# Optimization experiments

Measured on AMD Instinct MI355X. Metric: run time of the kernel, lower is better.

Reference implementation:

```python
import jax, jax.numpy as jnp
import numpy as np

NA, NW = 131072, 131072
N = NA + NW
E = 1048576
R = 4
DIN = 64
H = 128
L = 2
EPS = 1e-5


def setup_inputs() -> dict:
    key = jax.random.key(0)
    ks = jax.random.split(key, 20)
    s_in = 1.0 / np.sqrt(DIN)
    s_h = 1.0 / np.sqrt(H)
    return {
        "x_assignments": jax.random.normal(ks[0], (NA, DIN), jnp.float32),
        "x_workers": jax.random.normal(ks[1], (NW, DIN), jnp.float32),
        "edge_index": jax.random.randint(ks[2], (2, E), 0, N),
        "edge_type": jax.random.randint(ks[3], (E,), 0, R),
        "W_in_a": jax.random.normal(ks[4], (DIN, H), jnp.float32) * s_in,
        "b_in_a": jnp.zeros((H,), jnp.float32),
        "W_in_w": jax.random.normal(ks[5], (DIN, H), jnp.float32) * s_in,
        "b_in_w": jnp.zeros((H,), jnp.float32),
        "W_rel": jax.random.normal(ks[6], (L, R, H, H), jnp.float32) * s_h,
        "W_root": jax.random.normal(ks[7], (L, H, H), jnp.float32) * s_h,
        "b_conv": jnp.zeros((L, H), jnp.float32),
        "ln_g": jnp.ones((L, H), jnp.float32),
        "ln_b": jnp.zeros((L, H), jnp.float32),
        "W_out": jax.random.normal(ks[8], (H, 1), jnp.float32) * s_h,
        "b_out": jnp.zeros((1,), jnp.float32),
        "base": jnp.zeros((), jnp.float32),
    }


def _layernorm(x, g, b):
    mu = jnp.mean(x, axis=-1, keepdims=True)
    var = jnp.var(x, axis=-1, keepdims=True)
    return (x - mu) * jax.lax.rsqrt(var + EPS) * g + b


def reference(x_assignments, x_workers, edge_index, edge_type,
              W_in_a, b_in_a, W_in_w, b_in_w,
              W_rel, W_root, b_conv, ln_g, ln_b,
              W_out, b_out, base):
    # type-specific input projection + relu, then flatten node space
    ha = jax.nn.relu(x_assignments @ W_in_a + b_in_a)
    hw = jax.nn.relu(x_workers @ W_in_w + b_in_w)
    h = jnp.concatenate([ha, hw], axis=0)  # [N, H]
    src, dst = edge_index[0], edge_index[1]
    for l in range(L):
        hs = h[src]  # [E, H] gathered source features
        out = h @ W_root[l] + b_conv[l]  # root transform + bias
        for r in range(R):
            m = (edge_type == r).astype(h.dtype)  # [E]
            agg = jax.ops.segment_sum(hs * m[:, None], dst, num_segments=N)
            cnt = jax.ops.segment_sum(m, dst, num_segments=N)
            mean = agg / jnp.maximum(cnt, 1.0)[:, None]  # per-relation mean aggr
            out = out + mean @ W_rel[l, r]
        h = jax.nn.relu(_layernorm(out, ln_g[l], ln_b[l]))
        # dropout inactive (eval mode)
    h_t = h[:NA]  # target node type slice (offset 0)
    pred = base + (h_t @ W_out + b_out)[:, 0]
    return pred
```

## Files before the change

### kernel.cpp

```cpp
#include <hip/hip_runtime.h>

#define NA_ 131072
#define NN  262144
#define EE  1048576
#define RR  4
#define EPS_ 1e-5f

typedef unsigned short ushort_t;
typedef unsigned char uchar_t;
typedef unsigned int uint_t;
typedef __attribute__((ext_vector_type(8))) short bf16x8;
typedef __attribute__((ext_vector_type(4))) float f32x4;

__device__ __forceinline__ float bf2f(uint_t u16) {
    return __uint_as_float(u16 << 16);
}
__device__ __forceinline__ uint_t f2bf(float f) {
    uint_t x = __float_as_uint(f);
    return (x + 0x7fffu + ((x >> 16) & 1u)) >> 16;
}

__device__ __forceinline__ void gl2lds16(const void* g, void* l) {
    __builtin_amdgcn_global_load_lds(
        (const __attribute__((address_space(1))) void*)g,
        (__attribute__((address_space(3))) void*)l, 16, 0, 0);
}

__global__ __launch_bounds__(256) void proj_gemm(const float* __restrict__ A,
                                                 const short* __restrict__ Btg,
                                                 const float* __restrict__ bias,
                                                 ushort_t* __restrict__ C) {
    const int K = 64;
    __shared__ short As[128][K + 8];
    __shared__ short Bs[128][K + 8];
    const int tid  = threadIdx.x;
    const int lane = tid & 63;
    const int l15  = lane & 15;
    const int q    = lane >> 4;
    const int wv   = tid >> 6;
    const int wr   = (wv >> 1) * 64;
    const int wc   = (wv & 1) * 64;
    const size_t blockRow = (size_t)blockIdx.x * 128;

    #pragma unroll
    for (int it = 0; it < 4; it++) {
        int sidx = (it * 256 + tid) * 8;
        int row = sidx / K, col = sidx % K;
        const float* Ag = A + (blockRow + row) * K + col;
        float4 v0 = *(const float4*)Ag;
        float4 v1 = *(const float4*)(Ag + 4);
        uint4 u;
        u.x = f2bf(v0.x) | (f2bf(v0.y) << 16);
        u.y = f2bf(v0.z) | (f2bf(v0.w) << 16);
        u.z = f2bf(v1.x) | (f2bf(v1.y) << 16);
        u.w = f2bf(v1.z) | (f2bf(v1.w) << 16);
        *(uint4*)&As[row][col] = u;
        *(uint4*)&Bs[row][col] = *(const uint4*)(Btg + (size_t)row * K + col);
    }
    __syncthreads();

    f32x4 acc[4][4];
    #pragma unroll
    for (int i = 0; i < 4; i++)
        #pragma unroll
        for (int j = 0; j < 4; j++) {
            acc[i][j][0] = 0.f; acc[i][j][1] = 0.f;
            acc[i][j][2] = 0.f; acc[i][j][3] = 0.f;
        }

    #pragma unroll
    for (int kk = 0; kk < 2; kk++) {
        bf16x8 af[4], bfr[4];
        #pragma unroll
        for (int i = 0; i < 4; i++)
            af[i] = *(const bf16x8*)&As[wr + i * 16 + l15][kk * 32 + q * 8];
        #pragma unroll
        for (int j = 0; j < 4; j++)
            bfr[j] = *(const bf16x8*)&Bs[wc + j * 16 + l15][kk * 32 + q * 8];
        #pragma unroll
        for (int i = 0; i < 4; i++)
            #pragma unroll
            for (int j = 0; j < 4; j++)
                acc[i][j] = __builtin_amdgcn_mfma_f32_16x16x32_bf16(
                    af[i], bfr[j], acc[i][j], 0, 0, 0);
    }

    #pragma unroll
    for (int j = 0; j < 4; j++) {
        int gcol = wc + j * 16 + l15;
        float bv = bias[gcol];
        #pragma unroll
        for (int i = 0; i < 4; i++) {
            size_t rbase = blockRow + wr + i * 16 + q * 4;
            #pragma unroll
            for (int r = 0; r < 4; r++) {
                float v = fmaxf(acc[i][j][r] + bv, 0.f);
                C[(rbase + r) * 128 + gcol] = (ushort_t)f2bf(v);
            }
        }
    }
}

__global__ void prep_weights(const float* __restrict__ Wia,
                             const float* __restrict__ Wiw,
                             const float* __restrict__ Wroot,
                             const float* __restrict__ Wrel,
                             short* __restrict__ wt) {
    int e = blockIdx.x * 256 + threadIdx.x;
    if (e < 8192) {
        int k = e >> 7, n = e & 127;
        wt[n * 64 + k] = (short)f2bf(Wia[e]);
    } else if (e < 16384) {
        int t = e - 8192;
        int k = t >> 7, n = t & 127;
        wt[8192 + n * 64 + k] = (short)f2bf(Wiw[t]);
    } else {
        int t = e - 16384;
        int l = t / 81920;
        int d = t % 81920;
        int kc = d / 16384;
        int rem2 = d % 16384;
        int n = rem2 >> 7;
        int kkk = rem2 & 127;
        float val = (kc < 4)
            ? Wrel[(((size_t)l * 4 + kc) * 128 + kkk) * 128 + n]
            : Wroot[((size_t)l * 128 + kkk) * 128 + n];
        wt[16384 + (size_t)l * 81920 + kc * 16384 + n * 128 + kkk] =
            (short)f2bf(val);
    }
}

__global__ void count_edges(const int* __restrict__ dstv,
                            const int* __restrict__ et,
                            uint_t* __restrict__ cntp,
                            uchar_t* __restrict__ rank) {
    int base = blockIdx.x * 1024 + threadIdx.x;
    int e0 = base, e1 = base + 256, e2 = base + 512, e3 = base + 768;
    int r0 = et[e0], r1 = et[e1], r2 = et[e2], r3 = et[e3];
    int d0 = dstv[e0], d1 = dstv[e1], d2 = dstv[e2], d3 = dstv[e3];
    uint_t o0 = atomicAdd(&cntp[d0], 1u << (8 * r0));
    uint_t o1 = atomicAdd(&cntp[d1], 1u << (8 * r1));
    uint_t o2 = atomicAdd(&cntp[d2], 1u << (8 * r2));
    uint_t o3 = atomicAdd(&cntp[d3], 1u << (8 * r3));
    rank[e0] = (uchar_t)((o0 >> (8 * r0)) & 0xffu);
    rank[e1] = (uchar_t)((o1 >> (8 * r1)) & 0xffu);
    rank[e2] = (uchar_t)((o2 >> (8 * r2)) & 0xffu);
    rank[e3] = (uchar_t)((o3 >> (8 * r3)) & 0xffu);
}

__global__ void inv_deg(uint_t* __restrict__ cntp, float* __restrict__ inv,
                        int* __restrict__ deg) {
    int i = blockIdx.x * 256 + threadIdx.x;
    if (i < NN) {
        uint_t c = cntp[i];
        int c0 = c & 255, c1 = (c >> 8) & 255, c2 = (c >> 16) & 255, c3 = c >> 24;
        inv[i]          = 1.0f / (float)(c0 > 1 ? c0 : 1);
        inv[NN + i]     = 1.0f / (float)(c1 > 1 ? c1 : 1);
        inv[2 * NN + i] = 1.0f / (float)(c2 > 1 ? c2 : 1);
        inv[3 * NN + i] = 1.0f / (float)(c3 > 1 ? c3 : 1);
        deg[i] = c0 + c1 + c2 + c3;
        cntp[i] = ((uint_t)c0 << 8) | ((uint_t)(c0 + c1) << 16)
                | ((uint_t)(c0 + c1 + c2) << 24);
    }
}

__global__ void scan1(const int* __restrict__ deg, int* __restrict__ offs,
                      int* __restrict__ bsum) {
    __shared__ int lds[256];
    int tid = threadIdx.x;
    int i = blockIdx.x * 256 + tid;
    int v = deg[i];
    int incl = v;
    lds[tid] = incl;
    __syncthreads();
    for (int off = 1; off < 256; off <<= 1) {
        int t = (tid >= off) ? lds[tid - off] : 0;
        __syncthreads();
        incl += t;
        lds[tid] = incl;
        __syncthreads();
    }
    offs[i] = incl - v;
    if (tid == 255) bsum[blockIdx.x] = incl;
}

__global__ void scan_bsum(int* __restrict__ bsum) {
    __shared__ int lds[256];
    int tid = threadIdx.x;
    int t0 = bsum[tid * 4 + 0], t1 = bsum[tid * 4 + 1];
    int t2 = bsum[tid * 4 + 2], t3 = bsum[tid * 4 + 3];
    int s = t0 + t1 + t2 + t3;
    int incl = s;
    lds[tid] = incl;
    __syncthreads();
    for (int off = 1; off < 256; off <<= 1) {
        int t = (tid >= off) ? lds[tid - off] : 0;
        __syncthreads();
        incl += t;
        lds[tid] = incl;
        __syncthreads();
    }
    int e = incl - s;
    bsum[tid * 4 + 0] = e;
    bsum[tid * 4 + 1] = e + t0;
    bsum[tid * 4 + 2] = e + t0 + t1;
    bsum[tid * 4 + 3] = e + t0 + t1 + t2;
}

__global__ void scan_add(int* __restrict__ offs, const int* __restrict__ bsum) {
    int i = blockIdx.x * 256 + threadIdx.x;
    offs[i] = offs[i] + bsum[blockIdx.x];
    if (i == 0) offs[NN] = EE;
}

__global__ void place_edges(const int* __restrict__ srcv,
                            const int* __restrict__ dstv,
                            const int* __restrict__ et,
                            const uchar_t* __restrict__ rank,
                            const int* __restrict__ offs,
                            const uint_t* __restrict__ pref,
                            uint_t* __restrict__ pk) {
    int base = blockIdx.x * 1024 + threadIdx.x;
    #pragma unroll
    for (int t = 0; t < 4; t++) {
        int e = base + t * 256;
        int d = dstv[e], r = et[e];
        int pos = offs[d] + (int)((pref[d] >> (8 * r)) & 255u) + (int)rank[e];
        pk[pos] = (uint_t)srcv[e] | ((uint_t)r << 18);
    }
}

__global__ __launch_bounds__(256) void agg_means(const uint_t* __restrict__ pk,
                                                 const int* __restrict__ offs,
                                                 const ushort_t* __restrict__ hold,
                                                 const float* __restrict__ inv,
                                                 ushort_t* __restrict__ M,
                                                 int lo, int rowsCap) {
    int idx = blockIdx.x * 4 + (threadIdx.x >> 6);
    int d = lo + idx;
    int lane = threadIdx.x & 63;
    int beg = __builtin_amdgcn_readfirstlane(offs[d]);
    int end = __builtin_amdgcn_readfirstlane(offs[d + 1]);

    float a0x = 0.f, a0y = 0.f, a1x = 0.f, a1y = 0.f;
    float a2x = 0.f, a2y = 0.f, a3x = 0.f, a3y = 0.f;

    const uint_t* hold32 = (const uint_t*)hold;

    auto accs = [&](uint_t p, uint_t v, bool valid) {
        float x = bf2f(v & 0xffffu), y = bf2f(v >> 16);
        uint_t r = p >> 18;
        float m0 = (valid && r == 0u) ? 1.f : 0.f;
        float m1 = (valid && r == 1u) ? 1.f : 0.f;
        float m2 = (valid && r == 2u) ? 1.f : 0.f;
        float m3 = (valid && r == 3u) ? 1.f : 0.f;
        a0x += m0 * x;  a0y += m0 * y;
        a1x += m1 * x;  a1y += m1 * y;
        a2x += m2 * x;  a2y += m2 * y;
        a3x += m3 * x;  a3y += m3 * y;
    };

    for (int e = beg; e < end; e += 4) {
        int last = end - 1;
        int i1 = (e + 1 < end) ? e + 1 : last;
        int i2 = (e + 2 < end) ? e + 2 : last;
        int i3 = (e + 3 < end) ? e + 3 : last;
        uint_t p0 = pk[e];
        uint_t p1 = pk[i1];
        uint_t p2 = pk[i2];
        uint_t p3 = pk[i3];
        uint_t v0 = hold32[(size_t)(p0 & 0x3FFFFu) * 64 + lane];
        uint_t v1 = hold32[(size_t)(p1 & 0x3FFFFu) * 64 + lane];
        uint_t v2 = hold32[(size_t)(p2 & 0x3FFFFu) * 64 + lane];
        uint_t v3 = hold32[(size_t)(p3 & 0x3FFFFu) * 64 + lane];
        accs(p0, v0, true);
        accs(p1, v1, e + 1 < end);
        accs(p2, v2, e + 2 < end);
        accs(p3, v3, e + 3 < end);
    }

    float w0 = inv[d], w1 = inv[NN + d], w2 = inv[2 * NN + d], w3 = inv[3 * NN + d];
    uint_t* P = (uint_t*)M;
    size_t planeU = (size_t)rowsCap * 64;
    size_t rowU = (size_t)idx * 64 + lane;
    P[rowU]              = f2bf(a0x * w0) | (f2bf(a0y * w0) << 16);
    P[planeU + rowU]     = f2bf(a1x * w1) | (f2bf(a1y * w1) << 16);
    P[2 * planeU + rowU] = f2bf(a2x * w2) | (f2bf(a2y * w2) << 16);
    P[3 * planeU + rowU] = f2bf(a3x * w3) | (f2bf(a3y * w3) << 16);
}

template<bool HEAD>
__global__ __launch_bounds__(256) void layer_gemm_ln(
    const ushort_t* __restrict__ Mg,
    const ushort_t* __restrict__ hold,
    const short* __restrict__ Btg,
    const float* __restrict__ bconv,
    const float* __restrict__ lng,
    const float* __restrict__ lnb,
    ushort_t* __restrict__ hnew,
    const float* __restrict__ Wout,
    const float* __restrict__ bout,
    const float* __restrict__ basep,
    float* __restrict__ pred,
    int lo, int rowsCap) {
    __shared__ short As[64 * 128];
    __shared__ short Bs[128 * 128];
    __shared__ float lds_s[64][2], lds_q[64][2], lds_h[64][2];

    const int tid  = threadIdx.x;
    const int lane = tid & 63;
    const int l15  = lane & 15;
    const int q    = lane >> 4;
    const int wv   = tid >> 6;
    const int wr   = (wv >> 1) * 32;
    const int wc   = (wv & 1) * 64;
    const int blockRowL = blockIdx.x * 64;
    const size_t planeS = (size_t)rowsCap * 128;

    f32x4 acc[2][4];
    #pragma unroll
    for (int i = 0; i < 2; i++)
        #pragma unroll
        for (int j = 0; j < 4; j++) {
            acc[i][j][0] = 0.f; acc[i][j][1] = 0.f;
            acc[i][j][2] = 0.f; acc[i][j][3] = 0.f;
        }

    const int rloc = lane >> 4;
    const int gsw  = (lane & 15) ^ ((wv * 4 + rloc) & 15);
    const int lby  = (rloc << 8) + (gsw << 4);

    for (int kc = 0; kc < 5; kc++) {
        const char* asrc = (kc < 4)
            ? (const char*)(Mg + (size_t)kc * planeS + (size_t)blockRowL * 128)
            : (const char*)(hold + (size_t)(lo + blockRowL) * 128);
        const char* bsrc = (const char*)(Btg + (size_t)kc * 16384);
        __syncthreads();
        #pragma unroll
        for (int it = 0; it < 8; it++) {
            int off = it * 4096 + wv * 1024;
            if (it < 4) gl2lds16(asrc + off + lby, (char*)As + off);
            gl2lds16(bsrc + off + lby, (char*)Bs + off);
        }
        __syncthreads();

        #pragma unroll
        for (int kk = 0; kk < 4; kk++) {
            bf16x8 af[2], bfr[4];
            #pragma unroll
            for (int i = 0; i < 2; i++)
                af[i] = *(const bf16x8*)
                    &As[(wr + i * 16 + l15) * 128 + (((kk * 4 + q) ^ l15) << 3)];
            #pragma unroll
            for (int j = 0; j < 4; j++)
                bfr[j] = *(const bf16x8*)
                    &Bs[(wc + j * 16 + l15) * 128 + (((kk * 4 + q) ^ l15) << 3)];
            #pragma unroll
            for (int i = 0; i < 2; i++)
                #pragma unroll
                for (int j = 0; j < 4; j++)
                    acc[i][j] = __builtin_amdgcn_mfma_f32_16x16x32_bf16(
                        af[i], bfr[j], acc[i][j], 0, 0, 0);
        }
    }

    float bj[4], gj[4], bbj[4], wj[4];
    #pragma unroll
    for (int j = 0; j < 4; j++) {
        int col = wc + j * 16 + l15;
        bj[j]  = bconv[col];
        gj[j]  = lng[col];
        bbj[j] = lnb[col];
        if (HEAD) wj[j] = Wout[col];
    }
    #pragma unroll
    for (int i = 0; i < 2; i++)
        #pragma unroll
        for (int j = 0; j < 4; j++)
            #pragma unroll
            for (int r = 0; r < 4; r++) acc[i][j][r] += bj[j];

    float ps[2][4], pq[2][4];
    #pragma unroll
    for (int i = 0; i < 2; i++)
        #pragma unroll
        for (int r = 0; r < 4; r++) {
            float s = 0.f, qq = 0.f;
            #pragma unroll
            for (int j = 0; j < 4; j++) {
                float v = acc[i][j][r];
                s += v;
                qq += v * v;
            }
            ps[i][r] = s;
            pq[i][r] = qq;
        }
    #pragma unroll
    for (int m = 1; m <= 8; m <<= 1)
        #pragma unroll
        for (int i = 0; i < 2; i++)
            #pragma unroll
            for (int r = 0; r < 4; r++) {
                ps[i][r] += __shfl_xor(ps[i][r], m);
                pq[i][r] += __shfl_xor(pq[i][r], m);
            }

    if (l15 == 0) {
        #pragma unroll
        for (int i = 0; i < 2; i++)
            #pragma unroll
            for (int r = 0; r < 4; r++) {
                int row = wr + i * 16 + q * 4 + r;
                lds_s[row][wv & 1] = ps[i][r];
                lds_q[row][wv & 1] = pq[i][r];
            }
    }
    __syncthreads();

    float hs[2][4];
    #pragma unroll
    for (int i = 0; i < 2; i++)
        #pragma unroll
        for (int r = 0; r < 4; r++) {
            int row = wr + i * 16 + q * 4 + r;
            float sum = lds_s[row][0] + lds_s[row][1];
            float sq  = lds_q[row][0] + lds_q[row][1];
            float mu  = sum * (1.0f / 128.0f);
            float var = sq * (1.0f / 128.0f) - mu * mu;
            float rs  = rsqrtf(var + EPS_);
            size_t gr = (size_t)(lo + blockRowL + row) * 128;
            float hd = 0.f;
            #pragma unroll
            for (int j = 0; j < 4; j++) {
                float v = (acc[i][j][r] - mu) * rs * gj[j] + bbj[j];
                v = fmaxf(v, 0.f);
                if (HEAD) hd += v * wj[j];
                else hnew[gr + wc + j * 16 + l15] = (ushort_t)f2bf(v);
            }
            if (HEAD) hs[i][r] = hd;
        }

    if (HEAD) {
        #pragma unroll
        for (int m = 1; m <= 8; m <<= 1)
            #pragma unroll
            for (int i = 0; i < 2; i++)
                #pragma unroll
                for (int r = 0; r < 4; r++)
                    hs[i][r] += __shfl_xor(hs[i][r], m);
        if (l15 == 0) {
            #pragma unroll
            for (int i = 0; i < 2; i++)
                #pragma unroll
                for (int r = 0; r < 4; r++) {
                    int row = wr + i * 16 + q * 4 + r;
                    lds_h[row][wv & 1] = hs[i][r];
                }
        }
        __syncthreads();
        if (tid < 64)
            pred[lo + blockRowL + tid] =
                lds_h[tid][0] + lds_h[tid][1] + bout[0] + basep[0];
    }
}

extern "C" void kernel_launch(void* const* d_in, const int* in_sizes, int n_in,
                              void* d_out, int out_size, void* d_ws, size_t ws_size,
                              hipStream_t stream) {
    const float* x_a    = (const float*)d_in[0];
    const float* x_w    = (const float*)d_in[1];
    const int*   eidx   = (const int*)d_in[2];
    const int*   etype  = (const int*)d_in[3];
    const float* W_in_a = (const float*)d_in[4];
    const float* b_in_a = (const float*)d_in[5];
    const float* W_in_w = (const float*)d_in[6];
    const float* b_in_w = (const float*)d_in[7];
    const float* W_rel  = (const float*)d_in[8];
    const float* W_root = (const float*)d_in[9];
    const float* b_conv = (const float*)d_in[10];
    const float* ln_g   = (const float*)d_in[11];
    const float* ln_b   = (const float*)d_in[12];
    const float* W_out  = (const float*)d_in[13];
    const float* b_out  = (const float*)d_in[14];
    const float* base   = (const float*)d_in[15];

    const int* src  = eidx;
    const int* dstv = eidx + EE;

    char* p = (char*)d_ws;
    auto alloc = [&](size_t bytes) {
        char* q = p;
        p += (bytes + 255) & ~(size_t)255;
        return q;
    };
    ushort_t* hB   = (ushort_t*)alloc((size_t)NN * 128 * 2);
    float*    inv  = (float*)alloc((size_t)RR * NN * 4);
    uint_t*   pk   = (uint_t*)alloc((size_t)EE * 4);
    int*      offs = (int*)alloc((size_t)(NN + 1) * 4);
    short*    wbuf = (short*)alloc((size_t)180224 * 2);
    char*     hA_region = p;
    ushort_t* hA   = (ushort_t*)alloc((size_t)NN * 128 * 2);
    char*     scratch = p;
    uint_t*   cntp = (uint_t*)alloc((size_t)NN * 4);
    uchar_t*  rank = (uchar_t*)alloc((size_t)EE);
    int*      deg  = (int*)alloc((size_t)NN * 4);
    int*      bsum = (int*)alloc((size_t)1024 * 4);

    size_t rem0 = (ws_size > (size_t)(scratch - (char*)d_ws))
                      ? (ws_size - (size_t)(scratch - (char*)d_ws)) : 0;
    int cap0 = (int)(rem0 / 1024);
    if (cap0 > NN) cap0 = NN;
    cap0 &= ~127;
    if (cap0 == 0) cap0 = 128;
    size_t rem1 = (ws_size > (size_t)(hA_region - (char*)d_ws))
                      ? (ws_size - (size_t)(hA_region - (char*)d_ws)) : 0;
    int cap1 = (int)(rem1 / 1024);
    if (cap1 > NA_) cap1 = NA_;
    cap1 &= ~127;
    if (cap1 == 0) cap1 = 128;

    short* wt_ina = wbuf;
    short* wt_inw = wbuf + 8192;
    auto wt_layer = [&](int l) { return wbuf + 16384 + (size_t)l * 81920; };

    hipMemsetAsync(cntp, 0, (size_t)NN * sizeof(uint_t), stream);
    count_edges<<<EE / 1024, 256, 0, stream>>>(dstv, etype, cntp, rank);
    inv_deg<<<NN / 256, 256, 0, stream>>>(cntp, inv, deg);
    scan1<<<NN / 256, 256, 0, stream>>>(deg, offs, bsum);
    scan_bsum<<<1, 256, 0, stream>>>(bsum);
    scan_add<<<NN / 256, 256, 0, stream>>>(offs, bsum);
    place_edges<<<EE / 1024, 256, 0, stream>>>(src, dstv, etype, rank, offs,
                                               cntp, pk);

    prep_weights<<<704, 256, 0, stream>>>(W_in_a, W_in_w, W_root, W_rel, wbuf);

    proj_gemm<<<NA_ / 128, 256, 0, stream>>>(x_a, wt_ina, b_in_a, hA);
    proj_gemm<<<NA_ / 128, 256, 0, stream>>>(x_w, wt_inw, b_in_w,
                                             hA + (size_t)NA_ * 128);

    ushort_t* hc = hA;
    ushort_t* hn = hB;
    for (int l = 0; l < 2; l++) {
        int Nout = (l == 0) ? NN : NA_;
        ushort_t* M = (l == 0) ? (ushort_t*)scratch : (ushort_t*)hA_region;
        int cap = (l == 0) ? cap0 : cap1;
        int nch = (Nout + cap - 1) / cap;
        int chunk = ((Nout / nch) + 127) & ~127;
        if (chunk > cap) chunk = cap;
        for (int lo = 0; lo < Nout; lo += chunk) {
            int cr = (Nout - lo < chunk) ? (Nout - lo) : chunk;
            agg_means<<<cr / 4, 256, 0, stream>>>(pk, offs, hc, inv, M, lo,
                                                  cap);
            if (l == 0)
                layer_gemm_ln<false><<<cr / 64, 256, 0, stream>>>(
                    M, hc, wt_layer(l), b_conv + l * 128, ln_g + l * 128,
                    ln_b + l * 128, hn, nullptr, nullptr, nullptr, nullptr,
                    lo, cap);
            else
                layer_gemm_ln<true><<<cr / 64, 256, 0, stream>>>(
                    M, hc, wt_layer(l), b_conv + l * 128, ln_g + l * 128,
                    ln_b + l * 128, nullptr, W_out, b_out, base,
                    (float*)d_out, lo, cap);
        }
        ushort_t* t = hc; hc = hn; hn = t;
    }
}
```

Baseline: 511.5 us.

## Process two destination rows per wave in aggregation; pad edge counters and pack inverse degrees

The aggregation kernel now has each wavefront handle two destination nodes and interleaves their gathers, so more independent loads are in flight. When one node's edges are used up, the other is processed eight edges at a time. Per-node atomic counters are spread to one per 64 bytes to reduce contention between atomics on neighbouring counters. Inverse degrees are stored as a float4 per node so they load in one access, and the prefix counts go to a separate buffer. In exchange, the counter memset and its footprint grow 16x, and the scratch space left for aggregation chunks shrinks.

```diff
diff --git a/kernel.cpp b/kernel.cpp
--- a/kernel.cpp
+++ b/kernel.cpp
@@ -138,29 +138,33 @@
     int e0 = base, e1 = base + 256, e2 = base + 512, e3 = base + 768;
     int r0 = et[e0], r1 = et[e1], r2 = et[e2], r3 = et[e3];
     int d0 = dstv[e0], d1 = dstv[e1], d2 = dstv[e2], d3 = dstv[e3];
-    uint_t o0 = atomicAdd(&cntp[d0], 1u << (8 * r0));
-    uint_t o1 = atomicAdd(&cntp[d1], 1u << (8 * r1));
-    uint_t o2 = atomicAdd(&cntp[d2], 1u << (8 * r2));
-    uint_t o3 = atomicAdd(&cntp[d3], 1u << (8 * r3));
+    uint_t o0 = atomicAdd(&cntp[(size_t)d0 * 16], 1u << (8 * r0));
+    uint_t o1 = atomicAdd(&cntp[(size_t)d1 * 16], 1u << (8 * r1));
+    uint_t o2 = atomicAdd(&cntp[(size_t)d2 * 16], 1u << (8 * r2));
+    uint_t o3 = atomicAdd(&cntp[(size_t)d3 * 16], 1u << (8 * r3));
     rank[e0] = (uchar_t)((o0 >> (8 * r0)) & 0xffu);
     rank[e1] = (uchar_t)((o1 >> (8 * r1)) & 0xffu);
     rank[e2] = (uchar_t)((o2 >> (8 * r2)) & 0xffu);
     rank[e3] = (uchar_t)((o3 >> (8 * r3)) & 0xffu);
 }
 
-__global__ void inv_deg(uint_t* __restrict__ cntp, float* __restrict__ inv,
-                        int* __restrict__ deg) {
+__global__ void inv_deg(const uint_t* __restrict__ cntp,
+                        float* __restrict__ inv,
+                        int* __restrict__ deg,
+                        uint_t* __restrict__ prefd) {
     int i = blockIdx.x * 256 + threadIdx.x;
     if (i < NN) {
-        uint_t c = cntp[i];
+        uint_t c = cntp[(size_t)i * 16];
         int c0 = c & 255, c1 = (c >> 8) & 255, c2 = (c >> 16) & 255, c3 = c >> 24;
-        inv[i]          = 1.0f / (float)(c0 > 1 ? c0 : 1);
-        inv[NN + i]     = 1.0f / (float)(c1 > 1 ? c1 : 1);
-        inv[2 * NN + i] = 1.0f / (float)(c2 > 1 ? c2 : 1);
-        inv[3 * NN + i] = 1.0f / (float)(c3 > 1 ? c3 : 1);
+        float4 w;
+        w.x = 1.0f / (float)(c0 > 1 ? c0 : 1);
+        w.y = 1.0f / (float)(c1 > 1 ? c1 : 1);
+        w.z = 1.0f / (float)(c2 > 1 ? c2 : 1);
+        w.w = 1.0f / (float)(c3 > 1 ? c3 : 1);
+        ((float4*)inv)[i] = w;
         deg[i] = c0 + c1 + c2 + c3;
-        cntp[i] = ((uint_t)c0 << 8) | ((uint_t)(c0 + c1) << 16)
-                | ((uint_t)(c0 + c1 + c2) << 24);
+        prefd[i] = ((uint_t)c0 << 8) | ((uint_t)(c0 + c1) << 16)
+                 | ((uint_t)(c0 + c1 + c2) << 24);
     }
 }
 
@@ -218,17 +222,22 @@
                             const int* __restrict__ et,
                             const uchar_t* __restrict__ rank,
                             const int* __restrict__ offs,
-                            const uint_t* __restrict__ pref,
+                            const uint_t* __restrict__ prefd,
                             uint_t* __restrict__ pk) {
     int base = blockIdx.x * 1024 + threadIdx.x;
     #pragma unroll
     for (int t = 0; t < 4; t++) {
         int e = base + t * 256;
         int d = dstv[e], r = et[e];
-        int pos = offs[d] + (int)((pref[d] >> (8 * r)) & 255u) + (int)rank[e];
+        int pos = offs[d] + (int)((prefd[d] >> (8 * r)) & 255u) + (int)rank[e];
         pk[pos] = (uint_t)srcv[e] | ((uint_t)r << 18);
     }
 }
+
+struct Acc8 {
+    float a0x = 0.f, a0y = 0.f, a1x = 0.f, a1y = 0.f;
+    float a2x = 0.f, a2y = 0.f, a3x = 0.f, a3y = 0.f;
+};
 
 __global__ __launch_bounds__(256) void agg_means(const uint_t* __restrict__ pk,
                                                  const int* __restrict__ offs,
@@ -236,57 +245,108 @@
                                                  const float* __restrict__ inv,
                                                  ushort_t* __restrict__ M,
                                                  int lo, int rowsCap) {
-    int idx = blockIdx.x * 4 + (threadIdx.x >> 6);
-    int d = lo + idx;
-    int lane = threadIdx.x & 63;
-    int beg = __builtin_amdgcn_readfirstlane(offs[d]);
-    int end = __builtin_amdgcn_readfirstlane(offs[d + 1]);
-
-    float a0x = 0.f, a0y = 0.f, a1x = 0.f, a1y = 0.f;
-    float a2x = 0.f, a2y = 0.f, a3x = 0.f, a3y = 0.f;
+    const int wv   = __builtin_amdgcn_readfirstlane(threadIdx.x >> 6);
+    const int idx0 = blockIdx.x * 8 + wv * 2;
+    const int idx1 = idx0 + 1;
+    const int d0   = lo + idx0;
+    const int lane = threadIdx.x & 63;
+    const int b0   = offs[d0];
+    const int n0   = offs[d0 + 1];
+    const int n1   = offs[d0 + 2];
+    const float4 w40 = ((const float4*)inv)[d0];
+    const float4 w41 = ((const float4*)inv)[d0 + 1];
 
     const uint_t* hold32 = (const uint_t*)hold;
 
-    auto accs = [&](uint_t p, uint_t v, bool valid) {
+    Acc8 A0, A1;
+
+    auto accs = [&](Acc8& A, uint_t p, uint_t v, bool valid) {
         float x = bf2f(v & 0xffffu), y = bf2f(v >> 16);
         uint_t r = p >> 18;
         float m0 = (valid && r == 0u) ? 1.f : 0.f;
         float m1 = (valid && r == 1u) ? 1.f : 0.f;
         float m2 = (valid && r == 2u) ? 1.f : 0.f;
         float m3 = (valid && r == 3u) ? 1.f : 0.f;
-        a0x += m0 * x;  a0y += m0 * y;
-        a1x += m1 * x;  a1y += m1 * y;
-        a2x += m2 * x;  a2y += m2 * y;
-        a3x += m3 * x;  a3y += m3 * y;
+        A.a0x += m0 * x;  A.a0y += m0 * y;
+        A.a1x += m1 * x;  A.a1y += m1 * y;
+        A.a2x += m2 * x;  A.a2y += m2 * y;
+        A.a3x += m3 * x;  A.a3y += m3 * y;
     };
-
-    for (int e = beg; e < end; e += 4) {
-        int last = end - 1;
+    auto gather4 = [&](int e, int end, uint_t* p, uint_t* v) {
+        const int last = end - 1;
         int i1 = (e + 1 < end) ? e + 1 : last;
         int i2 = (e + 2 < end) ? e + 2 : last;
         int i3 = (e + 3 < end) ? e + 3 : last;
-        uint_t p0 = pk[e];
-        uint_t p1 = pk[i1];
-        uint_t p2 = pk[i2];
-        uint_t p3 = pk[i3];
-        uint_t v0 = hold32[(size_t)(p0 & 0x3FFFFu) * 64 + lane];
-        uint_t v1 = hold32[(size_t)(p1 & 0x3FFFFu) * 64 + lane];
-        uint_t v2 = hold32[(size_t)(p2 & 0x3FFFFu) * 64 + lane];
-        uint_t v3 = hold32[(size_t)(p3 & 0x3FFFFu) * 64 + lane];
-        accs(p0, v0, true);
-        accs(p1, v1, e + 1 < end);
-        accs(p2, v2, e + 2 < end);
-        accs(p3, v3, e + 3 < end);
-    }
-
-    float w0 = inv[d], w1 = inv[NN + d], w2 = inv[2 * NN + d], w3 = inv[3 * NN + d];
+        p[0] = pk[e];  p[1] = pk[i1];  p[2] = pk[i2];  p[3] = pk[i3];
+        v[0] = hold32[(size_t)(p[0] & 0x3FFFFu) * 64 + lane];
+        v[1] = hold32[(size_t)(p[1] & 0x3FFFFu) * 64 + lane];
+        v[2] = hold32[(size_t)(p[2] & 0x3FFFFu) * 64 + lane];
+        v[3] = hold32[(size_t)(p[3] & 0x3FFFFu) * 64 + lane];
+    };
+    auto acc4 = [&](Acc8& A, const uint_t* p, const uint_t* v, int e, int end) {
+        accs(A, p[0], v[0], true);
+        accs(A, p[1], v[1], e + 1 < end);
+        accs(A, p[2], v[2], e + 2 < end);
+        accs(A, p[3], v[3], e + 3 < end);
+    };
+
+    int e0 = b0, e1 = n0;
+    for (;;) {
+        const bool h0 = e0 < n0, h1 = e1 < n1;
+        if (h0 && h1) {
+            uint_t p0[4], v0[4], p1[4], v1[4];
+            gather4(e0, n0, p0, v0);
+            gather4(e1, n1, p1, v1);
+            acc4(A0, p0, v0, e0, n0);
+            acc4(A1, p1, v1, e1, n1);
+            e0 += 4; e1 += 4;
+        } else if (h0) {
+            uint_t p[4], v[4];
+            gather4(e0, n0, p, v);
+            if (e0 + 4 < n0) {
+                uint_t q[4], u[4];
+                gather4(e0 + 4, n0, q, u);
+                accs(A0, p[0], v[0], true);
+                accs(A0, p[1], v[1], true);
+                accs(A0, p[2], v[2], true);
+                accs(A0, p[3], v[3], true);
+                acc4(A0, q, u, e0 + 4, n0);
+            } else {
+                acc4(A0, p, v, e0, n0);
+            }
+            e0 += 8;
+        } else if (h1) {
+            uint_t p[4], v[4];
+            gather4(e1, n1, p, v);
+            if (e1 + 4 < n1) {
+                uint_t q[4], u[4];
+                gather4(e1 + 4, n1, q, u);
+                accs(A1, p[0], v[0], true);
+                accs(A1, p[1], v[1], true);
+                accs(A1, p[2], v[2], true);
+                accs(A1, p[3], v[3], true);
+                acc4(A1, q, u, e1 + 4, n1);
+            } else {
+                acc4(A1, p, v, e1, n1);
+            }
+            e1 += 8;
+        } else {
+            break;
+        }
+    }
+
     uint_t* P = (uint_t*)M;
     size_t planeU = (size_t)rowsCap * 64;
-    size_t rowU = (size_t)idx * 64 + lane;
-    P[rowU]              = f2bf(a0x * w0) | (f2bf(a0y * w0) << 16);
-    P[planeU + rowU]     = f2bf(a1x * w1) | (f2bf(a1y * w1) << 16);
-    P[2 * planeU + rowU] = f2bf(a2x * w2) | (f2bf(a2y * w2) << 16);
-    P[3 * planeU + rowU] = f2bf(a3x * w3) | (f2bf(a3y * w3) << 16);
+    size_t r0u = (size_t)idx0 * 64 + lane;
+    size_t r1u = (size_t)idx1 * 64 + lane;
+    P[r0u]              = f2bf(A0.a0x * w40.x) | (f2bf(A0.a0y * w40.x) << 16);
+    P[planeU + r0u]     = f2bf(A0.a1x * w40.y) | (f2bf(A0.a1y * w40.y) << 16);
+    P[2 * planeU + r0u] = f2bf(A0.a2x * w40.z) | (f2bf(A0.a2y * w40.z) << 16);
+    P[3 * planeU + r0u] = f2bf(A0.a3x * w40.w) | (f2bf(A0.a3y * w40.w) << 16);
+    P[r1u]              = f2bf(A1.a0x * w41.x) | (f2bf(A1.a0y * w41.x) << 16);
+    P[planeU + r1u]     = f2bf(A1.a1x * w41.y) | (f2bf(A1.a1y * w41.y) << 16);
+    P[2 * planeU + r1u] = f2bf(A1.a2x * w41.z) | (f2bf(A1.a2y * w41.z) << 16);
+    P[3 * planeU + r1u] = f2bf(A1.a3x * w41.w) | (f2bf(A1.a3y * w41.w) << 16);
 }
 
 template<bool HEAD>
@@ -501,10 +561,11 @@
     char*     hA_region = p;
     ushort_t* hA   = (ushort_t*)alloc((size_t)NN * 128 * 2);
     char*     scratch = p;
-    uint_t*   cntp = (uint_t*)alloc((size_t)NN * 4);
-    uchar_t*  rank = (uchar_t*)alloc((size_t)EE);
-    int*      deg  = (int*)alloc((size_t)NN * 4);
-    int*      bsum = (int*)alloc((size_t)1024 * 4);
+    uint_t*   cntp  = (uint_t*)alloc((size_t)NN * 64);
+    uchar_t*  rank  = (uchar_t*)alloc((size_t)EE);
+    int*      deg   = (int*)alloc((size_t)NN * 4);
+    uint_t*   prefd = (uint_t*)alloc((size_t)NN * 4);
+    int*      bsum  = (int*)alloc((size_t)1024 * 4);
 
     size_t rem0 = (ws_size > (size_t)(scratch - (char*)d_ws))
                       ? (ws_size - (size_t)(scratch - (char*)d_ws)) : 0;
@@ -523,14 +584,14 @@
     short* wt_inw = wbuf + 8192;
     auto wt_layer = [&](int l) { return wbuf + 16384 + (size_t)l * 81920; };
 
-    hipMemsetAsync(cntp, 0, (size_t)NN * sizeof(uint_t), stream);
+    hipMemsetAsync(cntp, 0, (size_t)NN * 64, stream);
     count_edges<<<EE / 1024, 256, 0, stream>>>(dstv, etype, cntp, rank);
-    inv_deg<<<NN / 256, 256, 0, stream>>>(cntp, inv, deg);
+    inv_deg<<<NN / 256, 256, 0, stream>>>(cntp, inv, deg, prefd);
     scan1<<<NN / 256, 256, 0, stream>>>(deg, offs, bsum);
     scan_bsum<<<1, 256, 0, stream>>>(bsum);
     scan_add<<<NN / 256, 256, 0, stream>>>(offs, bsum);
     place_edges<<<EE / 1024, 256, 0, stream>>>(src, dstv, etype, rank, offs,
-                                               cntp, pk);
+                                               prefd, pk);
 
     prep_weights<<<704, 256, 0, stream>>>(W_in_a, W_in_w, W_root, W_rel, wbuf);
 
@@ -549,7 +610,7 @@
         if (chunk > cap) chunk = cap;
         for (int lo = 0; lo < Nout; lo += chunk) {
             int cr = (Nout - lo < chunk) ? (Nout - lo) : chunk;
-            agg_means<<<cr / 4, 256, 0, stream>>>(pk, offs, hc, inv, M, lo,
+            agg_means<<<cr / 8, 256, 0, stream>>>(pk, offs, hc, inv, M, lo,
                                                   cap);
             if (l == 0)
                 layer_gemm_ln<false><<<cr / 64, 256, 0, stream>>>(
```

Result: no change. 509.3 us (-0.4%).
